# Kernel optimization log

Measured on AMD Instinct MI355X. Metric: run time of the kernel, lower is better.

Reference implementation:

```python
import jax, jax.numpy as jnp
import numpy as np

EPS = 1e-3  # matches epsilon=0.001

def setup_inputs() -> dict:
    key = jax.random.key(0)
    k1, k2, k3, k4 = jax.random.split(key, 4)
    B, T, D, K = 16, 512, 256, 8
    x = jax.random.normal(k1, (B, T, D), dtype=jnp.float32)
    # custom initializers: mean ~ U(-1,1), variance ~ U(0.001,0.01), prior ~ U(0.01,0.99) normalized
    mean = jax.random.uniform(k2, (K, D), minval=-1.0, maxval=1.0, dtype=jnp.float32)
    variance = jax.random.uniform(k3, (K, D), minval=0.001, maxval=0.01, dtype=jnp.float32)
    prior = jax.random.uniform(k4, (K, 1), minval=0.01, maxval=0.99, dtype=jnp.float32)
    prior = prior / jnp.sum(prior, axis=0)
    return {"x": x, "mean": mean, "variance": variance, "prior": prior}

def reference(x, mean, variance, prior):
    # x: [B,T,D]; mean/variance: [K,D]; prior: [K,1]
    var = jax.nn.softplus(variance)                    # [K,D]
    pr = jax.nn.softmax(prior, axis=-1)                # [K,1] (softmax over size-1 axis -> ones; faithful)
    pr_k = pr[:, 0][:, None, None, None]               # [K,1,1,1]
    diff = x[None] - mean[:, None, None, :]            # [K,B,T,D]
    p = pr_k * jnp.exp(-0.5 * diff * diff / (var[:, None, None, :] + EPS))  # [K,B,T,D]
    denom = jnp.sum(p, axis=0)                         # [B,T,D]
    tau = p / (denom[None] + EPS)                      # [K,B,T,D]
    sum_tau = jnp.sum(tau, axis=(1, 2), keepdims=True) # [K,1,1,D] (sum over B,T)
    hat_tau = tau / (sum_tau + EPS)
    prod = hat_tau * x                                 # [K,B,T,D]
    expectation = jnp.mean(prod, axis=2, keepdims=True)         # [K,B,1,D]
    v = x[None] - expectation                                    # [K,B,T,D]
    var_kb = jnp.mean(hat_tau * prod * prod, axis=2, keepdims=True)  # [K,B,1,D]
    hat_x_k = v / jnp.sqrt(var_kb + EPS)
    out = jnp.sum(tau / jnp.sqrt(pr_k + EPS) * hat_x_k, axis=0)  # [B,T,D]
    return out
```

## Files before the change

### kernel.cpp

```cpp
#include <hip/hip_runtime.h>


namespace {
constexpr int K = 8, B = 16, T = 512, D = 256;
constexpr float EPS = 1e-3f;
constexpr int DSL = 16;
constexpr int NSL = D / DSL;
constexpr int TCH = 2;
constexpr int TLC = T / TCH;
constexpr int TP  = 16;
constexpr int RT  = TLC / TP;
constexpr int KS  = 3 * K;
constexpr int PSZ = TCH * K * B * D;
}

__global__ __launch_bounds__(256) void ucb_k1(
    const float* __restrict__ x, const float* __restrict__ mean,
    const float* __restrict__ variance,
    float* __restrict__ pt, float* __restrict__ p1s, float* __restrict__ p3s)
{
  __shared__ float red[TP][DSL][KS + 1];

  const int tid = threadIdx.x;
  const int dl  = tid & 15;
  const int tp  = tid >> 4;
  const int bi  = blockIdx.x;
  const int b   = bi >> 5;
  const int sl  = (bi >> 1) & 15;
  const int tch = bi & 1;
  const int dd  = sl*DSL + dl;

  float qa[K], qb[K], qc[K];
#pragma unroll
  for (int k = 0; k < K; ++k) {
    float mk = mean[k*D + dd];
    float sp = log1pf(__expf(variance[k*D + dd]));
    float nh = -0.5f / (sp + EPS);
    qa[k] = nh; qb[k] = -2.0f*nh*mk; qc[k] = nh*mk*mk;
  }

  float ast[K], as1[K], as3[K];
#pragma unroll
  for (int k = 0; k < K; ++k) { ast[k]=0.f; as1[k]=0.f; as3[k]=0.f; }

  const float* xp = x + ((size_t)b*T + (size_t)tch*TLC + tp)*D + dd;
#pragma unroll 4
  for (int j = 0; j < RT; ++j) {
    float xv = xp[(size_t)j*TP*D];
    float x2 = xv*xv;
    float p[K];
#pragma unroll
    for (int k = 0; k < K; ++k)
      p[k] = __expf(fmaf(qa[k], x2, fmaf(qb[k], xv, qc[k])));
    float den = EPS + ((p[0]+p[1])+(p[2]+p[3])) + ((p[4]+p[5])+(p[6]+p[7]));
    float rden = __builtin_amdgcn_rcpf(den);
#pragma unroll
    for (int k = 0; k < K; ++k) {
      float tau = p[k]*rden;
      float tx  = tau*xv;
      ast[k] += tau;
      as1[k] += tx;
      as3[k]  = fmaf(tx*tx, tau, as3[k]);
    }
  }

#pragma unroll
  for (int k = 0; k < K; ++k) {
    red[tp][dl][3*k+0] = ast[k];
    red[tp][dl][3*k+1] = as1[k];
    red[tp][dl][3*k+2] = as3[k];
  }
  __syncthreads();

#pragma unroll
  for (int i = 0; i < 2; ++i) {
    const int item = tid + i*256;
    if (item < DSL*KS) {
      const int dloc = item / KS;
      const int ks   = item % KS;
      float s = 0.f;
#pragma unroll
      for (int t2 = 0; t2 < TP; ++t2) s += red[t2][dloc][ks];
      const int k = ks / 3, stat = ks % 3;
      const size_t idx = ((size_t)((tch*K + k)*B + b))*D + sl*DSL + dloc;
      if      (stat == 0) pt [idx] = s;
      else if (stat == 1) p1s[idx] = s;
      else                p3s[idx] = s;
    }
  }
}

__global__ __launch_bounds__(256) void ucb_fin(
    const float* __restrict__ pt, const float* __restrict__ p1s,
    const float* __restrict__ p3s, float* __restrict__ er)
{
  __shared__ float reds[B][17];

  const int k  = blockIdx.x >> 4;
  const int d0 = (blockIdx.x & 15) * 16;
  const int dl = threadIdx.x & 15;
  const int bb = threadIdx.x >> 4;
  const int d  = d0 + dl;

  const size_t i0 = ((size_t)(k*B + bb))*D + d;
  const size_t i1 = i0 + (size_t)K*B*D;
  const float a0 = pt [i0] + pt [i1];
  const float a1 = p1s[i0] + p1s[i1];
  const float a3 = p3s[i0] + p3s[i1];

  reds[bb][dl] = a0;
  __syncthreads();
  if (threadIdx.x < 16) {
    float s = 0.f;
#pragma unroll
    for (int b2 = 0; b2 < B; ++b2) s += reds[b2][threadIdx.x];
    reds[0][threadIdx.x] = 1.0f / (s + EPS);
  }
  __syncthreads();

  const float rS = reds[0][dl];
  const float rT = 1.0f / T;
  const float e  = a1 * rT * rS;
  const float vv = a3 * rT * (rS*rS*rS);
  const float r  = rsqrtf(vv + EPS);
  er[((size_t)(bb*K + k)*2 + 0)*D + d] = e;
  er[((size_t)(bb*K + k)*2 + 1)*D + d] = r;
}

__global__ __launch_bounds__(256) void ucb_k2(
    const float* __restrict__ x, const float* __restrict__ mean,
    const float* __restrict__ variance, const float* __restrict__ er,
    float* __restrict__ out)
{
  const int d  = threadIdx.x;
  const int b  = blockIdx.x >> 6;
  const int tc = blockIdx.x & 63;

  float qa[K], qb[K], qc[K], rr[K], erc[K];
#pragma unroll
  for (int k = 0; k < K; ++k) {
    float mk = mean[k*D + d];
    float sp = log1pf(__expf(variance[k*D + d]));
    float nh = -0.5f / (sp + EPS);
    qa[k] = nh; qb[k] = -2.0f*nh*mk; qc[k] = nh*mk*mk;
    float e = er[((size_t)(b*K + k)*2 + 0)*D + d];
    float r = er[((size_t)(b*K + k)*2 + 1)*D + d];
    rr[k] = r; erc[k] = e*r;
  }

  const float isp = 0.99950037f;
  const size_t base = ((size_t)b*T + (size_t)tc*8)*D + d;
#pragma unroll
  for (int t = 0; t < 8; ++t) {
    float xv = x[base + (size_t)t*D];
    float x2 = xv*xv;
    float p[K];
#pragma unroll
    for (int k = 0; k < K; ++k)
      p[k] = __expf(fmaf(qa[k], x2, fmaf(qb[k], xv, qc[k])));
    float den = EPS + ((p[0]+p[1])+(p[2]+p[3])) + ((p[4]+p[5])+(p[6]+p[7]));
    float rden = __builtin_amdgcn_rcpf(den);
    float acc1 = 0.f, acc2 = 0.f;
#pragma unroll
    for (int k = 0; k < K; ++k) {
      acc1 = fmaf(p[k], rr[k],  acc1);
      acc2 = fmaf(p[k], erc[k], acc2);
    }
    out[base + (size_t)t*D] = (xv*acc1 - acc2) * rden * isp;
  }
}

extern "C" void kernel_launch(void* const* d_in, const int* in_sizes, int n_in,
                              void* d_out, int out_size, void* d_ws, size_t ws_size,
                              hipStream_t stream) {
  const float* x        = (const float*)d_in[0];
  const float* mean     = (const float*)d_in[1];
  const float* variance = (const float*)d_in[2];

  float* out = (float*)d_out;
  float* w   = (float*)d_ws;
  float* pt  = w;
  float* p1s = pt  + PSZ;
  float* p3s = p1s + PSZ;
  float* er  = p3s + PSZ;

  ucb_k1 <<<B*NSL*TCH, 256, 0, stream>>>(x, mean, variance, pt, p1s, p3s);
  ucb_fin<<<K*(D/16),  256, 0, stream>>>(pt, p1s, p3s, er);
  ucb_k2 <<<B*64,      256, 0, stream>>>(x, mean, variance, er, out);
}
```

Before: 85.50 us.

## Fuse finalize kernel into second pass, recomputing per-batch statistics in LDS

Removes the separate ucb_fin launch and its er round trip. Each ucb_k2 block now reduces the partial sums itself, including summing pt over all B and both T-chunks, and keeps r and e*r in shared memory. The second pass now runs 256 blocks of 512 threads, each covering 32 timesteps, instead of 1024 blocks covering 8. This saves a launch and a global sync, but every block redundantly does 2048 x 32 extra pt reads, and fewer blocks may reduce latency hiding.

Measured after the change: 87.63 us. 2.5% more time.

```diff
diff --git a/kernel.cpp b/kernel.cpp
--- a/kernel.cpp
+++ b/kernel.cpp
@@ -90,51 +90,46 @@
   }
 }
 
-__global__ __launch_bounds__(256) void ucb_fin(
+__global__ __launch_bounds__(512) void ucb_k2(
+    const float* __restrict__ x, const float* __restrict__ mean,
+    const float* __restrict__ variance,
     const float* __restrict__ pt, const float* __restrict__ p1s,
-    const float* __restrict__ p3s, float* __restrict__ er)
+    const float* __restrict__ p3s, float* __restrict__ out)
 {
-  __shared__ float reds[B][17];
+  __shared__ float rr_l[K][D];
+  __shared__ float erc_l[K][D];
 
-  const int k  = blockIdx.x >> 4;
-  const int d0 = (blockIdx.x & 15) * 16;
-  const int dl = threadIdx.x & 15;
-  const int bb = threadIdx.x >> 4;
-  const int d  = d0 + dl;
+  const int tid = threadIdx.x;
+  const int b   = blockIdx.x >> 4;
+  const int tc  = blockIdx.x & 15;
 
-  const size_t i0 = ((size_t)(k*B + bb))*D + d;
-  const size_t i1 = i0 + (size_t)K*B*D;
-  const float a0 = pt [i0] + pt [i1];
-  const float a1 = p1s[i0] + p1s[i1];
-  const float a3 = p3s[i0] + p3s[i1];
-
-  reds[bb][dl] = a0;
-  __syncthreads();
-  if (threadIdx.x < 16) {
-    float s = 0.f;
+  const float rT = 1.0f / T;
 #pragma unroll
-    for (int b2 = 0; b2 < B; ++b2) s += reds[b2][threadIdx.x];
-    reds[0][threadIdx.x] = 1.0f / (s + EPS);
+  for (int i = 0; i < 4; ++i) {
+    const int item = tid + i*512;
+    const int d = item & 255;
+    const int k = item >> 8;
+    float S = EPS;
+#pragma unroll
+    for (int tch = 0; tch < TCH; ++tch)
+#pragma unroll
+      for (int bb = 0; bb < B; ++bb)
+        S += pt[((size_t)((tch*K + k)*B + bb))*D + d];
+    const size_t i0 = ((size_t)((0*K + k)*B + b))*D + d;
+    const size_t i1 = ((size_t)((1*K + k)*B + b))*D + d;
+    const float a1 = p1s[i0] + p1s[i1];
+    const float a3 = p3s[i0] + p3s[i1];
+    const float rS = 1.0f / S;
+    const float e  = a1 * rT * rS;
+    const float vv = a3 * rT * (rS*rS*rS);
+    const float r  = rsqrtf(vv + EPS);
+    rr_l[k][d]  = r;
+    erc_l[k][d] = e * r;
   }
   __syncthreads();
 
-  const float rS = reds[0][dl];
-  const float rT = 1.0f / T;
-  const float e  = a1 * rT * rS;
-  const float vv = a3 * rT * (rS*rS*rS);
-  const float r  = rsqrtf(vv + EPS);
-  er[((size_t)(bb*K + k)*2 + 0)*D + d] = e;
-  er[((size_t)(bb*K + k)*2 + 1)*D + d] = r;
-}
-
-__global__ __launch_bounds__(256) void ucb_k2(
-    const float* __restrict__ x, const float* __restrict__ mean,
-    const float* __restrict__ variance, const float* __restrict__ er,
-    float* __restrict__ out)
-{
-  const int d  = threadIdx.x;
-  const int b  = blockIdx.x >> 6;
-  const int tc = blockIdx.x & 63;
+  const int d  = tid & 255;
+  const int t2 = tid >> 8;
 
   float qa[K], qb[K], qc[K], rr[K], erc[K];
 #pragma unroll
@@ -143,16 +138,15 @@
     float sp = log1pf(__expf(variance[k*D + d]));
     float nh = -0.5f / (sp + EPS);
     qa[k] = nh; qb[k] = -2.0f*nh*mk; qc[k] = nh*mk*mk;
-    float e = er[((size_t)(b*K + k)*2 + 0)*D + d];
-    float r = er[((size_t)(b*K + k)*2 + 1)*D + d];
-    rr[k] = r; erc[k] = e*r;
+    rr[k]  = rr_l[k][d];
+    erc[k] = erc_l[k][d];
   }
 
   const float isp = 0.99950037f;
-  const size_t base = ((size_t)b*T + (size_t)tc*8)*D + d;
-#pragma unroll
-  for (int t = 0; t < 8; ++t) {
-    float xv = x[base + (size_t)t*D];
+  const size_t base = ((size_t)b*T + (size_t)tc*32 + t2)*D + d;
+#pragma unroll 4
+  for (int j = 0; j < 16; ++j) {
+    float xv = x[base + (size_t)(j*2)*D];
     float x2 = xv*xv;
     float p[K];
 #pragma unroll
@@ -166,7 +160,7 @@
       acc1 = fmaf(p[k], rr[k],  acc1);
       acc2 = fmaf(p[k], erc[k], acc2);
     }
-    out[base + (size_t)t*D] = (xv*acc1 - acc2) * rden * isp;
+    out[base + (size_t)(j*2)*D] = (xv*acc1 - acc2) * rden * isp;
   }
 }
 
@@ -182,9 +176,7 @@
   float* pt  = w;
   float* p1s = pt  + PSZ;
   float* p3s = p1s + PSZ;
-  float* er  = p3s + PSZ;
 
-  ucb_k1 <<<B*NSL*TCH, 256, 0, stream>>>(x, mean, variance, pt, p1s, p3s);
-  ucb_fin<<<K*(D/16),  256, 0, stream>>>(pt, p1s, p3s, er);
-  ucb_k2 <<<B*64,      256, 0, stream>>>(x, mean, variance, er, out);
+  ucb_k1<<<B*NSL*TCH, 256, 0, stream>>>(x, mean, variance, pt, p1s, p3s);
+  ucb_k2<<<B*16,      512, 0, stream>>>(x, mean, variance, pt, p1s, p3s, out);
 }
```
